# Kernel optimization log

Hardware: AMD Instinct MI355X
Metric: run time of the kernel (lower is better)

## Reference

```python
import jax, jax.numpy as jnp
import numpy as np

H = 16
D_MODEL = 1024
D_K = D_MODEL // H
B, S = 2, 2048


def setup_inputs() -> dict:
    key = jax.random.key(0)
    ks = jax.random.split(key, 11)
    scale = 1.0 / np.sqrt(D_MODEL)
    inp = {
        "query": jax.random.normal(ks[0], (B, S, D_MODEL), jnp.float32),
        "key": jax.random.normal(ks[1], (B, S, D_MODEL), jnp.float32),
        "value": jax.random.normal(ks[2], (B, S, D_MODEL), jnp.float32),
        # four nn.Linear(d_model, d_model): Wq, Wk, Wv, Wo (torch convention: y = x @ W.T + b)
        "Wq": jax.random.uniform(ks[3], (D_MODEL, D_MODEL), jnp.float32, -scale, scale),
        "bq": jax.random.uniform(ks[4], (D_MODEL,), jnp.float32, -scale, scale),
        "Wk": jax.random.uniform(ks[5], (D_MODEL, D_MODEL), jnp.float32, -scale, scale),
        "bk": jax.random.uniform(ks[6], (D_MODEL,), jnp.float32, -scale, scale),
        "Wv": jax.random.uniform(ks[7], (D_MODEL, D_MODEL), jnp.float32, -scale, scale),
        "bv": jax.random.uniform(ks[8], (D_MODEL,), jnp.float32, -scale, scale),
        "Wo": jax.random.uniform(ks[9], (D_MODEL, D_MODEL), jnp.float32, -scale, scale),
        "bo": jax.random.uniform(ks[10], (D_MODEL,), jnp.float32, -scale, scale),
    }
    return inp


def _split_heads(x):
    # [B, S, D] -> [B, H, S, d_k]
    b, s, _ = x.shape
    return x.reshape(b, s, H, D_K).transpose(0, 2, 1, 3)


def reference(query, key, value, Wq, bq, Wk, bk, Wv, bv, Wo, bo):
    q = _split_heads(query @ Wq.T + bq)
    k = _split_heads(key @ Wk.T + bk)
    v = _split_heads(value @ Wv.T + bv)
    # scaled dot-product attention (dropout omitted: reference is eval-mode)
    scores = jnp.einsum("bhqd,bhkd->bhqk", q, k) / np.sqrt(D_K).astype(np.float32)
    p = jax.nn.softmax(scores, axis=-1)
    x = jnp.einsum("bhqk,bhkd->bhqd", p, v)
    x = x.transpose(0, 2, 1, 3).reshape(query.shape[0], -1, H * D_K)
    return x @ Wo.T + bo
```

## Files before the change

### kernel.cpp

```cpp
#include <hip/hip_runtime.h>

typedef unsigned short u16;
typedef unsigned int u32;
typedef __attribute__((ext_vector_type(8))) short short8;
typedef __attribute__((ext_vector_type(8))) _Float16 half8;
typedef __attribute__((ext_vector_type(4))) float floatx4;
typedef __attribute__((ext_vector_type(4))) unsigned short ushortx4;
typedef __attribute__((ext_vector_type(4))) unsigned int uint4v;

#define DEV static __device__ __forceinline__

DEV float bf2f(u16 u) { union { unsigned u; float f; } v; v.u = ((unsigned)u) << 16; return v.f; }
DEV u16 f2bf(float f) {
  union { float f; unsigned u; } v; v.f = f;
  return (u16)((v.u + 0x7FFFu + ((v.u >> 16) & 1u)) >> 16);
}
DEV u16 f2h(float f) { return __builtin_bit_cast(u16, (_Float16)f); }
DEV u32 pkh(float a, float b) {
  return __builtin_bit_cast(u32, __builtin_amdgcn_cvt_pkrtz(a, b));
}
DEV float fexp2(float x) { return __builtin_amdgcn_exp2f(x); }

#define GLDS(g, l) __builtin_amdgcn_global_load_lds( \
    (const __attribute__((address_space(1))) void*)(g), \
    (__attribute__((address_space(3))) void*)(l), 16, 0, 0)

struct CvtArg {
  const float* src[11];
  u16* dst[11];
  int cum[12];
};

__global__ void convert(CvtArg a) {
  const long base = ((long)blockIdx.x * 256 + threadIdx.x) * 4;
  if (base >= a.cum[11]) return;
  int s = 0;
  while (s < 10 && base >= a.cum[s + 1]) ++s;
  const long off = base - a.cum[s];
  const float* sp = a.src[s] + off;
  ushortx4 u;
#pragma unroll
  for (int r = 0; r < 4; ++r) u[r] = f2bf(sp[r]);
  *(ushortx4*)(a.dst[s] + off) = u;
}

struct GemmArg {
  const u16* x;
  const u16* w;
  const u16* bias;
  u16* dst;
  int mode;
};

__global__ __launch_bounds__(256, 2) void gemm_nt(GemmArg g0, GemmArg g1, GemmArg g2) {
  GemmArg g = (blockIdx.z == 0) ? g0 : ((blockIdx.z == 1) ? g1 : g2);
  __shared__ u16 As[128 * 32];
  __shared__ u16 Bs[128 * 32];
  const int tid = threadIdx.x, w = tid >> 6, l = tid & 63;
  const int l15 = l & 15, quad = l >> 4;
  const int bm = blockIdx.x, bn = blockIdx.y;
  const int wm = w >> 1, wn = w & 1;

  floatx4 acc[4][4];
#pragma unroll
  for (int i = 0; i < 4; ++i)
#pragma unroll
    for (int j = 0; j < 4; ++j) acc[i][j] = (floatx4){0.f, 0.f, 0.f, 0.f};

  const u16* xb = g.x + (long)(bm * 128 + w * 16 + (l >> 2)) * 1024 + (l & 3) * 8;
  const u16* wb = g.w + (long)(bn * 128 + w * 16 + (l >> 2)) * 1024 + (l & 3) * 8;
  u16* asb = &As[(w * 16) * 32];
  u16* bsb = &Bs[(w * 16) * 32];

  for (int kt = 0; kt < 32; ++kt) {
    const int k0 = kt * 32;
    __syncthreads();
#pragma unroll
    for (int p = 0; p < 2; ++p) {
      GLDS(xb + (long)p * 64 * 1024 + k0, asb + p * 64 * 32);
      GLDS(wb + (long)p * 64 * 1024 + k0, bsb + p * 64 * 32);
    }
    __syncthreads();
    short8 af[4], bfr[4];
#pragma unroll
    for (int mi = 0; mi < 4; ++mi)
      af[mi] = *(const short8*)&As[(wm * 64 + mi * 16 + l15) * 32 + quad * 8];
#pragma unroll
    for (int ni = 0; ni < 4; ++ni)
      bfr[ni] = *(const short8*)&Bs[(wn * 64 + ni * 16 + l15) * 32 + quad * 8];
#pragma unroll
    for (int mi = 0; mi < 4; ++mi)
#pragma unroll
      for (int ni = 0; ni < 4; ++ni)
        acc[mi][ni] = __builtin_amdgcn_mfma_f32_16x16x32_bf16(af[mi], bfr[ni], acc[mi][ni], 0, 0, 0);
  }

  float bv[4];
#pragma unroll
  for (int ni = 0; ni < 4; ++ni) bv[ni] = bf2f(g.bias[bn * 128 + wn * 64 + ni * 16 + l15]);

#pragma unroll
  for (int mi = 0; mi < 4; ++mi) {
    const int mbase = bm * 128 + wm * 64 + mi * 16 + quad * 4;
#pragma unroll
    for (int ni = 0; ni < 4; ++ni) {
      const int n = bn * 128 + wn * 64 + ni * 16 + l15;
      if (g.mode == 2) {
        const int b = mbase >> 11, s = mbase & 2047;
        const int h = n >> 6, d = n & 63;
        ushortx4 u;
#pragma unroll
        for (int r = 0; r < 4; ++r) u[r] = f2h(acc[mi][ni][r] + bv[ni]);
        *(ushortx4*)&g.dst[((long)(b * 16 + h) * 64 + d) * 2048 + s] = u;
      } else if (g.mode == 3) {
        float* df = (float*)g.dst;
#pragma unroll
        for (int r = 0; r < 4; ++r)
          df[(long)(mbase + r) * 1024 + n] = acc[mi][ni][r] + bv[ni];
      } else {
        const float sc = (g.mode == 0) ? 0.18033688011f : 1.0f;
        const int h = n >> 6, d = n & 63;
#pragma unroll
        for (int r = 0; r < 4; ++r) {
          const int m = mbase + r, b = m >> 11, s = m & 2047;
          g.dst[((long)(b * 16 + h) * 2048 + s) * 64 + d] = f2bf((acc[mi][ni][r] + bv[ni]) * sc);
        }
      }
    }
  }
}

__global__ __launch_bounds__(256, 2) void attn_flash(const u16* __restrict__ Q,
                                                     const u16* __restrict__ K,
                                                     const u16* __restrict__ V,
                                                     u16* __restrict__ X) {
  __shared__ u16 KVs[4][64 * 72];
  const int tid = threadIdx.x, w = tid >> 6, l = tid & 63;
  const int l15 = l & 15, quad = l >> 4;
  const int qh = w >> 1, kh = w & 1;

  const int bid = blockIdx.x;
  const int xcd = bid & 7, idx = bid >> 3;
  const int qx = idx & 15, bh = xcd + 8 * (idx >> 4);
  const int q0 = qx * 128;

  const u16* qp = Q + (long)bh * 2048 * 64;
  const u16* kp = K + (long)bh * 2048 * 64;
  const u16* vp = V + (long)bh * 2048 * 64;

  const int r0 = tid >> 3, c0 = tid & 7, r1 = 32 + (tid >> 3);

  short8 skA0, svA0, skA1, svA1, skB0, svB0, skB1, svB1;

#define ISSUE_LOADS_A(kv0) \
    skA0 = *(const short8*)(kp + (long)((kv0) + r0) * 64 + c0 * 8); \
    svA0 = *(const short8*)(vp + (long)r0 * 2048 + (kv0) + c0 * 8); \
    skA1 = *(const short8*)(kp + (long)((kv0) + r1) * 64 + c0 * 8); \
    svA1 = *(const short8*)(vp + (long)r1 * 2048 + (kv0) + c0 * 8);

#define ISSUE_LOADS_B(kv0) \
    skB0 = *(const short8*)(kp + (long)((kv0) + r0) * 64 + c0 * 8); \
    svB0 = *(const short8*)(vp + (long)r0 * 2048 + (kv0) + c0 * 8); \
    skB1 = *(const short8*)(kp + (long)((kv0) + r1) * 64 + c0 * 8); \
    svB1 = *(const short8*)(vp + (long)r1 * 2048 + (kv0) + c0 * 8);

#define STORE_TILE_A(pb_) \
    *(short8*)&KVs[pb_][r0 * 72 + c0 * 8] = skA0; \
    *(short8*)&KVs[2 + (pb_)][r0 * 72 + c0 * 8] = svA0; \
    *(short8*)&KVs[pb_][r1 * 72 + c0 * 8] = skA1; \
    *(short8*)&KVs[2 + (pb_)][r1 * 72 + c0 * 8] = svA1;

#define STORE_TILE_B(pb_) \
    *(short8*)&KVs[pb_][r0 * 72 + c0 * 8] = skB0; \
    *(short8*)&KVs[2 + (pb_)][r0 * 72 + c0 * 8] = svB0; \
    *(short8*)&KVs[pb_][r1 * 72 + c0 * 8] = skB1; \
    *(short8*)&KVs[2 + (pb_)][r1 * 72 + c0 * 8] = svB1;

  short8 qf[4][2];
#pragma unroll
  for (int nq = 0; nq < 4; ++nq)
#pragma unroll
    for (int kc = 0; kc < 2; ++kc)
      qf[nq][kc] = *(const short8*)(qp + (long)(q0 + qh * 64 + nq * 16 + l15) * 64 + kc * 32 + quad * 8);

  floatx4 o[4][4];
#pragma unroll
  for (int nq = 0; nq < 4; ++nq)
#pragma unroll
    for (int nd = 0; nd < 4; ++nd) o[nq][nd] = (floatx4){0.f, 0.f, 0.f, 0.f};
  float den[4] = {0.f, 0.f, 0.f, 0.f};

  const bool p1 = (l & 32) != 0;
  const bool p3 = (l & 16) != 0;
  const bool p2 = p1 ^ p3;

#define BFLY(pbv, m00, m01, m10, m11) { \
    u32 A0 = p1 ? (m10) : (m00), A1 = p1 ? (m11) : (m01); \
    u32 s0_ = p1 ? (m00) : (m10), s1_ = p1 ? (m01) : (m11); \
    u32 B0 = (u32)__shfl_xor((int)s0_, 32), B1 = (u32)__shfl_xor((int)s1_, 32); \
    u32 t0 = p2 ? A0 : B0, t1 = p2 ? A1 : B1; \
    u32 u0 = (u32)__shfl_xor((int)t0, 16), u1 = (u32)__shfl_xor((int)t1, 16); \
    u32 w0 = p2 ? B0 : A0, w1 = p2 ? B1 : A1; \
    pbv[0] = p3 ? u0 : w0; pbv[1] = p3 ? u1 : w1; \
    pbv[2] = p3 ? w0 : u0; pbv[3] = p3 ? w1 : u1; \
  }

#define ATTN_ITER(t, p, IS, ST) { \
    if ((t) < 30) { IS(((t) + 2) * 64) } \
    if ((t) < 31) { ST((p) ^ 1) } \
    const int kr0 = kh * 32 + l15, kr1 = kh * 32 + 16 + l15; \
    short8 ak00 = *(const short8*)&KVs[p][kr0 * 72 + quad * 8]; \
    short8 ak01 = *(const short8*)&KVs[p][kr0 * 72 + 32 + quad * 8]; \
    short8 ak10 = *(const short8*)&KVs[p][kr1 * 72 + quad * 8]; \
    short8 ak11 = *(const short8*)&KVs[p][kr1 * 72 + 32 + quad * 8]; \
    half8 vf0 = *(const half8*)&KVs[2 + (p)][(0 * 16 + l15) * 72 + kh * 32 + quad * 8]; \
    half8 vf1 = *(const half8*)&KVs[2 + (p)][(1 * 16 + l15) * 72 + kh * 32 + quad * 8]; \
    half8 vf2 = *(const half8*)&KVs[2 + (p)][(2 * 16 + l15) * 72 + kh * 32 + quad * 8]; \
    half8 vf3 = *(const half8*)&KVs[2 + (p)][(3 * 16 + l15) * 72 + kh * 32 + quad * 8]; \
    u32 pk[4][2][2]; \
    _Pragma("unroll") \
    for (int nq = 0; nq < 4; ++nq) { \
      floatx4 st0 = (floatx4){0.f, 0.f, 0.f, 0.f}, st1 = (floatx4){0.f, 0.f, 0.f, 0.f}; \
      st0 = __builtin_amdgcn_mfma_f32_16x16x32_bf16(ak00, qf[nq][0], st0, 0, 0, 0); \
      st0 = __builtin_amdgcn_mfma_f32_16x16x32_bf16(ak01, qf[nq][1], st0, 0, 0, 0); \
      st1 = __builtin_amdgcn_mfma_f32_16x16x32_bf16(ak10, qf[nq][0], st1, 0, 0, 0); \
      st1 = __builtin_amdgcn_mfma_f32_16x16x32_bf16(ak11, qf[nq][1], st1, 0, 0, 0); \
      float e0 = fexp2(st0[0]), e1 = fexp2(st0[1]), e2 = fexp2(st0[2]), e3 = fexp2(st0[3]); \
      den[nq] += (e0 + e1) + (e2 + e3); \
      pk[nq][0][0] = pkh(e0, e1); pk[nq][0][1] = pkh(e2, e3); \
      e0 = fexp2(st1[0]); e1 = fexp2(st1[1]); e2 = fexp2(st1[2]); e3 = fexp2(st1[3]); \
      den[nq] += (e0 + e1) + (e2 + e3); \
      pk[nq][1][0] = pkh(e0, e1); pk[nq][1][1] = pkh(e2, e3); \
    } \
    _Pragma("unroll") \
    for (int nq = 0; nq < 4; ++nq) { \
      uint4v pb; \
      BFLY(pb, pk[nq][0][0], pk[nq][0][1], pk[nq][1][0], pk[nq][1][1]) \
      half8 pbs = __builtin_bit_cast(half8, pb); \
      o[nq][0] = __builtin_amdgcn_mfma_f32_16x16x32_f16(vf0, pbs, o[nq][0], 0, 0, 0); \
      o[nq][1] = __builtin_amdgcn_mfma_f32_16x16x32_f16(vf1, pbs, o[nq][1], 0, 0, 0); \
      o[nq][2] = __builtin_amdgcn_mfma_f32_16x16x32_f16(vf2, pbs, o[nq][2], 0, 0, 0); \
      o[nq][3] = __builtin_amdgcn_mfma_f32_16x16x32_f16(vf3, pbs, o[nq][3], 0, 0, 0); \
    } \
    __syncthreads(); \
  }

  ISSUE_LOADS_A(0)
  STORE_TILE_A(0)
  ISSUE_LOADS_B(64)
  __syncthreads();

  for (int tt = 0; tt < 32; tt += 2) {
    ATTN_ITER(tt, 0, ISSUE_LOADS_A, STORE_TILE_B)
    ATTN_ITER(tt + 1, 1, ISSUE_LOADS_B, STORE_TILE_A)
  }

  float dsum[4];
#pragma unroll
  for (int nq = 0; nq < 4; ++nq) {
    float d = den[nq];
    d += __shfl_xor(d, 16);
    d += __shfl_xor(d, 32);
    dsum[nq] = d;
  }

  float* osc = (float*)KVs;
  float* dsc = osc + 8192;
  if (kh == 1) {
#pragma unroll
    for (int nq = 0; nq < 4; ++nq)
#pragma unroll
      for (int nd = 0; nd < 4; ++nd)
        *(floatx4*)&osc[(((qh * 4 + nq) * 4 + nd) * 64 + l) * 4] = o[nq][nd];
    if (l < 16) {
#pragma unroll
      for (int nq = 0; nq < 4; ++nq) dsc[(qh * 4 + nq) * 16 + l] = dsum[nq];
    }
  }
  __syncthreads();

  if (kh == 0) {
    float rcp[4];
#pragma unroll
    for (int nq = 0; nq < 4; ++nq) rcp[nq] = 1.0f / (dsum[nq] + dsc[(qh * 4 + nq) * 16 + l15]);
    const int b = bh >> 4, h = bh & 15;
#pragma unroll
    for (int nq = 0; nq < 4; ++nq) {
      const int s = q0 + qh * 64 + nq * 16 + l15;
      u16* xrow = X + ((long)(b * 2048 + s)) * 1024 + h * 64;
#pragma unroll
      for (int nd = 0; nd < 4; ++nd) {
        floatx4 om = o[nq][nd] + *(const floatx4*)&osc[(((qh * 4 + nq) * 4 + nd) * 64 + l) * 4];
        ushortx4 u;
#pragma unroll
        for (int r = 0; r < 4; ++r) u[r] = f2bf(om[r] * rcp[nq]);
        *(ushortx4*)&xrow[nd * 16 + quad * 4] = u;
      }
    }
  }
}

extern "C" void kernel_launch(void* const* d_in, const int* in_sizes, int n_in,
                              void* d_out, int out_size, void* d_ws, size_t ws_size,
                              hipStream_t stream) {
  u16* ws = (u16*)d_ws;
  const size_t M1 = 1048576, M4 = 4194304;
  u16* NQ  = ws;
  u16* NK  = ws + M4;
  u16* NV  = ws + 2 * M4;
  u16* NWQ = ws + 3 * M4;
  u16* NWK = ws + 3 * M4 + M1;
  u16* NWV = ws + 3 * M4 + 2 * M1;
  u16* NWO = ws + 3 * M4 + 3 * M1;
  u16* NBQ = ws + 3 * M4 + 4 * M1;
  u16* NBK = NBQ + 1024;
  u16* NBV = NBQ + 2048;
  u16* NBO = NBQ + 3072;
  u16* Qb = ws + 16 * M1 + 8192;
  u16* Kb = Qb + M4;
  u16* Vb = Qb + 2 * M4;
  u16* Xb = NQ;

  CvtArg ca;
  u16* dsts[11] = {NQ, NK, NV, NWQ, NBQ, NWK, NBK, NWV, NBV, NWO, NBO};
  int sizes[11] = {(int)M4, (int)M4, (int)M4, (int)M1, 1024, (int)M1, 1024, (int)M1, 1024, (int)M1, 1024};
  int c = 0;
  for (int i = 0; i < 11; ++i) {
    ca.src[i] = (const float*)d_in[i];
    ca.dst[i] = dsts[i];
    ca.cum[i] = c;
    c += sizes[i];
  }
  ca.cum[11] = c;
  convert<<<(c / 4 + 255) / 256, 256, 0, stream>>>(ca);

  GemmArg gq{NQ, NWQ, NBQ, Qb, 0};
  GemmArg gk{NK, NWK, NBK, Kb, 1};
  GemmArg gv{NV, NWV, NBV, Vb, 2};
  gemm_nt<<<dim3(32, 8, 3), 256, 0, stream>>>(gq, gk, gv);

  attn_flash<<<dim3(512), 256, 0, stream>>>(Qb, Kb, Vb, Xb);

  GemmArg go{Xb, NWO, NBO, (u16*)d_out, 3};
  gemm_nt<<<dim3(32, 8, 1), 256, 0, stream>>>(go, go, go);
}
```

Measured before the change: 227.9 us.

## Fuse fp32-to-bf16 conversion into GEMM loads and retile output projection

```diff
diff --git a/kernel.cpp b/kernel.cpp
--- a/kernel.cpp
+++ b/kernel.cpp
@@ -19,46 +19,36 @@
 DEV u32 pkh(float a, float b) {
   return __builtin_bit_cast(u32, __builtin_amdgcn_cvt_pkrtz(a, b));
 }
+DEV u32 pkbf(float a, float b) {
+  union { float f; u32 u; } x, y; x.f = a; y.f = b;
+  return __builtin_amdgcn_perm(y.u + 0x8000u, x.u + 0x8000u, 0x07060302u);
+}
 DEV float fexp2(float x) { return __builtin_amdgcn_exp2f(x); }
 
 #define GLDS(g, l) __builtin_amdgcn_global_load_lds( \
     (const __attribute__((address_space(1))) void*)(g), \
     (__attribute__((address_space(3))) void*)(l), 16, 0, 0)
 
-struct CvtArg {
-  const float* src[11];
-  u16* dst[11];
-  int cum[12];
-};
-
-__global__ void convert(CvtArg a) {
-  const long base = ((long)blockIdx.x * 256 + threadIdx.x) * 4;
-  if (base >= a.cum[11]) return;
-  int s = 0;
-  while (s < 10 && base >= a.cum[s + 1]) ++s;
-  const long off = base - a.cum[s];
-  const float* sp = a.src[s] + off;
-  ushortx4 u;
-#pragma unroll
-  for (int r = 0; r < 4; ++r) u[r] = f2bf(sp[r]);
-  *(ushortx4*)(a.dst[s] + off) = u;
-}
-
 struct GemmArg {
-  const u16* x;
-  const u16* w;
-  const u16* bias;
+  const float* x;
+  const float* w;
+  const float* bias;
   u16* dst;
   int mode;
 };
 
-__global__ __launch_bounds__(256, 2) void gemm_nt(GemmArg g0, GemmArg g1, GemmArg g2) {
-  GemmArg g = (blockIdx.z == 0) ? g0 : ((blockIdx.z == 1) ? g1 : g2);
+__global__ __launch_bounds__(256, 2) void gemm_qkv(GemmArg g0, GemmArg g1, GemmArg g2) {
+  const int bid = blockIdx.x;
+  const int gidx = (bid & 7) * 96 + (bid >> 3);
+  const int bm = gidx & 31;
+  const int bnz = gidx >> 5;
+  const int bn = bnz & 7, z = bnz >> 3;
+  GemmArg g = (z == 0) ? g0 : ((z == 1) ? g1 : g2);
+
   __shared__ u16 As[128 * 32];
   __shared__ u16 Bs[128 * 32];
   const int tid = threadIdx.x, w = tid >> 6, l = tid & 63;
   const int l15 = l & 15, quad = l >> 4;
-  const int bm = blockIdx.x, bn = blockIdx.y;
   const int wm = w >> 1, wn = w & 1;
 
   floatx4 acc[4][4];
@@ -67,18 +57,24 @@
 #pragma unroll
     for (int j = 0; j < 4; ++j) acc[i][j] = (floatx4){0.f, 0.f, 0.f, 0.f};
 
-  const u16* xb = g.x + (long)(bm * 128 + w * 16 + (l >> 2)) * 1024 + (l & 3) * 8;
-  const u16* wb = g.w + (long)(bn * 128 + w * 16 + (l >> 2)) * 1024 + (l & 3) * 8;
-  u16* asb = &As[(w * 16) * 32];
-  u16* bsb = &Bs[(w * 16) * 32];
+  const float* xr = g.x + (long)(bm * 128 + w * 16 + (l >> 2)) * 1024 + (l & 3) * 8;
+  const float* wr = g.w + (long)(bn * 128 + w * 16 + (l >> 2)) * 1024 + (l & 3) * 8;
+  u16* asd = &As[(w * 16 + (l >> 2)) * 32 + (l & 3) * 8];
+  u16* bsd = &Bs[(w * 16 + (l >> 2)) * 32 + (l & 3) * 8];
 
   for (int kt = 0; kt < 32; ++kt) {
     const int k0 = kt * 32;
     __syncthreads();
 #pragma unroll
     for (int p = 0; p < 2; ++p) {
-      GLDS(xb + (long)p * 64 * 1024 + k0, asb + p * 64 * 32);
-      GLDS(wb + (long)p * 64 * 1024 + k0, bsb + p * 64 * 32);
+      floatx4 a0 = *(const floatx4*)(xr + (long)p * 64 * 1024 + k0);
+      floatx4 a1 = *(const floatx4*)(xr + (long)p * 64 * 1024 + k0 + 4);
+      floatx4 b0 = *(const floatx4*)(wr + (long)p * 64 * 1024 + k0);
+      floatx4 b1 = *(const floatx4*)(wr + (long)p * 64 * 1024 + k0 + 4);
+      uint4v da = {pkbf(a0[0], a0[1]), pkbf(a0[2], a0[3]), pkbf(a1[0], a1[1]), pkbf(a1[2], a1[3])};
+      uint4v db = {pkbf(b0[0], b0[1]), pkbf(b0[2], b0[3]), pkbf(b1[0], b1[1]), pkbf(b1[2], b1[3])};
+      *(uint4v*)(asd + p * 64 * 32) = da;
+      *(uint4v*)(bsd + p * 64 * 32) = db;
     }
     __syncthreads();
     short8 af[4], bfr[4];
@@ -97,7 +93,7 @@
 
   float bv[4];
 #pragma unroll
-  for (int ni = 0; ni < 4; ++ni) bv[ni] = bf2f(g.bias[bn * 128 + wn * 64 + ni * 16 + l15]);
+  for (int ni = 0; ni < 4; ++ni) bv[ni] = g.bias[bn * 128 + wn * 64 + ni * 16 + l15];
 
 #pragma unroll
   for (int mi = 0; mi < 4; ++mi) {
@@ -112,11 +108,6 @@
 #pragma unroll
         for (int r = 0; r < 4; ++r) u[r] = f2h(acc[mi][ni][r] + bv[ni]);
         *(ushortx4*)&g.dst[((long)(b * 16 + h) * 64 + d) * 2048 + s] = u;
-      } else if (g.mode == 3) {
-        float* df = (float*)g.dst;
-#pragma unroll
-        for (int r = 0; r < 4; ++r)
-          df[(long)(mbase + r) * 1024 + n] = acc[mi][ni][r] + bv[ni];
       } else {
         const float sc = (g.mode == 0) ? 0.18033688011f : 1.0f;
         const int h = n >> 6, d = n & 63;
@@ -126,6 +117,75 @@
           g.dst[((long)(b * 16 + h) * 2048 + s) * 64 + d] = f2bf((acc[mi][ni][r] + bv[ni]) * sc);
         }
       }
+    }
+  }
+}
+
+__global__ __launch_bounds__(256, 2) void gemm_o(const u16* __restrict__ x,
+                                                 const float* __restrict__ wo,
+                                                 const float* __restrict__ bias,
+                                                 float* __restrict__ dst) {
+  const int bid = blockIdx.x;
+  const int gidx = (bid & 7) * 64 + (bid >> 3);
+  const int bm = gidx & 63;
+  const int bn = gidx >> 6;
+
+  __shared__ u16 As[64 * 32];
+  __shared__ u16 Bs[128 * 32];
+  const int tid = threadIdx.x, w = tid >> 6, l = tid & 63;
+  const int l15 = l & 15, quad = l >> 4;
+  const int wm = w >> 1, wn = w & 1;
+
+  floatx4 acc[2][4];
+#pragma unroll
+  for (int i = 0; i < 2; ++i)
+#pragma unroll
+    for (int j = 0; j < 4; ++j) acc[i][j] = (floatx4){0.f, 0.f, 0.f, 0.f};
+
+  const u16* xb = x + (long)(bm * 64 + w * 16 + (l >> 2)) * 1024 + (l & 3) * 8;
+  const float* wr = wo + (long)(bn * 128 + w * 16 + (l >> 2)) * 1024 + (l & 3) * 8;
+  u16* asb = &As[(w * 16) * 32];
+  u16* bsd = &Bs[(w * 16 + (l >> 2)) * 32 + (l & 3) * 8];
+
+  for (int kt = 0; kt < 32; ++kt) {
+    const int k0 = kt * 32;
+    __syncthreads();
+    GLDS(xb + k0, asb);
+#pragma unroll
+    for (int p = 0; p < 2; ++p) {
+      floatx4 b0 = *(const floatx4*)(wr + (long)p * 64 * 1024 + k0);
+      floatx4 b1 = *(const floatx4*)(wr + (long)p * 64 * 1024 + k0 + 4);
+      uint4v db = {pkbf(b0[0], b0[1]), pkbf(b0[2], b0[3]), pkbf(b1[0], b1[1]), pkbf(b1[2], b1[3])};
+      *(uint4v*)(bsd + p * 64 * 32) = db;
+    }
+    __syncthreads();
+    short8 af[2], bfr[4];
+#pragma unroll
+    for (int mi = 0; mi < 2; ++mi)
+      af[mi] = *(const short8*)&As[(wm * 32 + mi * 16 + l15) * 32 + quad * 8];
+#pragma unroll
+    for (int ni = 0; ni < 4; ++ni)
+      bfr[ni] = *(const short8*)&Bs[(wn * 64 + ni * 16 + l15) * 32 + quad * 8];
+#pragma unroll
+    for (int mi = 0; mi < 2; ++mi)
+#pragma unroll
+      for (int ni = 0; ni < 4; ++ni)
+        acc[mi][ni] = __builtin_amdgcn_mfma_f32_16x16x32_bf16(af[mi], bfr[ni], acc[mi][ni], 0, 0, 0);
+  }
+
+  float bv[4];
+#pragma unroll
+  for (int ni = 0; ni < 4; ++ni) bv[ni] = bias[bn * 128 + wn * 64 + ni * 16 + l15];
+
+#pragma unroll
+  for (int mi = 0; mi < 2; ++mi) {
+    const int mbase = bm * 64 + wm * 32 + mi * 16 + quad * 4;
+#pragma unroll
+    for (int ni = 0; ni < 4; ++ni) {
+      const int n = bn * 128 + wn * 64 + ni * 16 + l15;
+#pragma unroll
+      for (int r = 0; r < 4; ++r)
+        dst[(long)(mbase + r) * 1024 + n] = acc[mi][ni][r] + bv[ni];
     }
   }
 }
@@ -304,43 +364,19 @@
                               void* d_out, int out_size, void* d_ws, size_t ws_size,
                               hipStream_t stream) {
   u16* ws = (u16*)d_ws;
-  const size_t M1 = 1048576, M4 = 4194304;
-  u16* NQ  = ws;
-  u16* NK  = ws + M4;
-  u16* NV  = ws + 2 * M4;
-  u16* NWQ = ws + 3 * M4;
-  u16* NWK = ws + 3 * M4 + M1;
-  u16* NWV = ws + 3 * M4 + 2 * M1;
-  u16* NWO = ws + 3 * M4 + 3 * M1;
-  u16* NBQ = ws + 3 * M4 + 4 * M1;
-  u16* NBK = NBQ + 1024;
-  u16* NBV = NBQ + 2048;
-  u16* NBO = NBQ + 3072;
-  u16* Qb = ws + 16 * M1 + 8192;
-  u16* Kb = Qb + M4;
-  u16* Vb = Qb + 2 * M4;
-  u16* Xb = NQ;
-
-  CvtArg ca;
-  u16* dsts[11] = {NQ, NK, NV, NWQ, NBQ, NWK, NBK, NWV, NBV, NWO, NBO};
-  int sizes[11] = {(int)M4, (int)M4, (int)M4, (int)M1, 1024, (int)M1, 1024, (int)M1, 1024, (int)M1, 1024};
-  int c = 0;
-  for (int i = 0; i < 11; ++i) {
-    ca.src[i] = (const float*)d_in[i];
-    ca.dst[i] = dsts[i];
-    ca.cum[i] = c;
-    c += sizes[i];
-  }
-  ca.cum[11] = c;
-  convert<<<(c / 4 + 255) / 256, 256, 0, stream>>>(ca);
-
-  GemmArg gq{NQ, NWQ, NBQ, Qb, 0};
-  GemmArg gk{NK, NWK, NBK, Kb, 1};
-  GemmArg gv{NV, NWV, NBV, Vb, 2};
-  gemm_nt<<<dim3(32, 8, 3), 256, 0, stream>>>(gq, gk, gv);
+  const size_t M4 = 4194304;
+  u16* Qb = ws;
+  u16* Kb = ws + M4;
+  u16* Vb = ws + 2 * M4;
+  u16* Xb = ws + 3 * M4;
+
+  GemmArg gq{(const float*)d_in[0], (const float*)d_in[3], (const float*)d_in[4], Qb, 0};
+  GemmArg gk{(const float*)d_in[1], (const float*)d_in[5], (const float*)d_in[6], Kb, 1};
+  GemmArg gv{(const float*)d_in[2], (const float*)d_in[7], (const float*)d_in[8], Vb, 2};
+  gemm_qkv<<<dim3(768), 256, 0, stream>>>(gq, gk, gv);
 
   attn_flash<<<dim3(512), 256, 0, stream>>>(Qb, Kb, Vb, Xb);
 
-  GemmArg go{Xb, NWO, NBO, (u16*)d_out, 3};
-  gemm_nt<<<dim3(32, 8, 1), 256, 0, stream>>>(go, go, go);
-}
+  gemm_o<<<dim3(512), 256, 0, stream>>>(Xb, (const float*)d_in[9], (const float*)d_in[10],
+                                        (float*)d_out);
+}
```

Result: slower. 270.5 us (+18.7%).
